# Kernel tuning notes

Measured on AMD Instinct MI355X. Metric: run time of the kernel, lower is better.

Reference implementation:

```python
import jax, jax.numpy as jnp
import numpy as np

PERIOD = 64
SCALE = 0.45


def setup_inputs() -> dict:
    key = jax.random.key(0)
    kq, kk, kv = jax.random.split(key, 3)
    B, L, D = 16, 8192, 512
    q = jax.random.normal(kq, (B, L, D), dtype=jnp.float32)
    k = jax.random.normal(kk, (B, L, D), dtype=jnp.float32)
    v = jax.random.normal(kv, (B, L, D), dtype=jnp.float32)
    return {"q": q, "k": k, "v": v}


def reference(q, k, v):
    # q, k, v: [B, L, D] with L % PERIOD == 0 and L == S, so the padding /
    # length-matching branches of the torch module are no-ops.
    B, L, D = q.shape
    nblk = L // PERIOD
    # permute to [B, D, L] then chunk the sequence into blocks of size PERIOD:
    # [B, D, nblk, PERIOD]. Attention is computed ACROSS blocks, with the
    # period dimension acting as the feature dimension.
    qb = q.transpose(0, 2, 1).reshape(B, D, nblk, PERIOD)
    kb = k.transpose(0, 2, 1).reshape(B, D, nblk, PERIOD)
    vb = v.transpose(0, 2, 1).reshape(B, D, nblk, PERIOD)
    # attn: [B, D, nblk, nblk]
    attn = jax.nn.softmax(jnp.einsum('bdnp,bdmp->bdnm', qb, kb) * SCALE, axis=-1)
    # out: [B, D, nblk, PERIOD] -> [B, D, L] -> [B, L, D]
    out = jnp.einsum('bdnm,bdmp->bdnp', attn, vb)
    out = out.reshape(B, D, L).transpose(0, 2, 1)
    return (out, attn)
```

## Files before the change

### kernel.cpp

```cpp
#include <hip/hip_runtime.h>
#include <stdint.h>

#define BB 16
#define LSEQ 8192
#define DD 512
#define PER 64
#define NBLK 128
#define QSCALE 0.45f

typedef __attribute__((ext_vector_type(8))) short short8;
typedef __attribute__((ext_vector_type(4))) float f32x4;
typedef __attribute__((ext_vector_type(2))) unsigned int uint2v;
typedef unsigned short ushort_t;

__device__ __forceinline__ ushort_t f2bf(float f) {
    union { float f; uint32_t u; } c; c.f = f;
    uint32_t u = c.u + 0x7FFFu + ((c.u >> 16) & 1u);
    return (ushort_t)(u >> 16);
}
__device__ __forceinline__ float bf2f(ushort_t h) {
    union { float f; uint32_t u; } c; c.u = ((uint32_t)h) << 16;
    return c.f;
}
__device__ __forceinline__ uint32_t pk2(float a, float b) {
    return (uint32_t)f2bf(a) | ((uint32_t)f2bf(b) << 16);
}

__global__ __launch_bounds__(256) void ktr(const float* __restrict__ q,
                                           const float* __restrict__ k,
                                           const float* __restrict__ v,
                                           ushort_t* __restrict__ qT,
                                           ushort_t* __restrict__ kT,
                                           ushort_t* __restrict__ vTT) {
    const int t = threadIdx.x;
    const int zz = blockIdx.z;
    const int role = zz >> 4;
    const int b = zz & (BB - 1);
    if (role < 2) {
        const float scale = role ? 1.0f : QSCALE;
        const float* sp = (role ? k : q) + (size_t)b * LSEQ * DD;
        ushort_t* dp = (role ? kT : qT) + (size_t)b * DD * LSEQ;
        const int l0 = blockIdx.x * 64 + 4 * (t & 15);
        const int d0 = blockIdx.y * 64 + 4 * (t >> 4);
        f32x4 vv[4];
#pragma unroll
        for (int j = 0; j < 4; ++j)
            vv[j] = __builtin_nontemporal_load(
                (const f32x4*)(sp + (size_t)(l0 + j) * DD + d0));
#pragma unroll
        for (int dj = 0; dj < 4; ++dj) {
            uint2v w;
            w[0] = pk2(vv[0][dj] * scale, vv[1][dj] * scale);
            w[1] = pk2(vv[2][dj] * scale, vv[3][dj] * scale);
            *(uint2v*)(dp + (size_t)(d0 + dj) * LSEQ + l0) = w;
        }
    } else {
        const int p = blockIdx.x & 63;
        const int mh = blockIdx.x >> 6;
        const int m0 = mh * 64 + 4 * (t & 15);
        const int d0 = blockIdx.y * 64 + 4 * (t >> 4);
        const float* vp = v + (size_t)b * LSEQ * DD;
        f32x4 x[4];
#pragma unroll
        for (int mj = 0; mj < 4; ++mj)
            x[mj] = __builtin_nontemporal_load(
                (const f32x4*)(vp + (size_t)((m0 + mj) * PER + p) * DD + d0));
#pragma unroll
        for (int dj = 0; dj < 4; ++dj) {
            uint2v w;
            w[0] = pk2(x[0][dj], x[1][dj]);
            w[1] = pk2(x[2][dj], x[3][dj]);
            *(uint2v*)(vTT + (size_t)((size_t)(b * DD + d0 + dj) * PER + p) * NBLK + m0) = w;
        }
    }
}

__global__ __launch_bounds__(256, 3) void katt(const ushort_t* __restrict__ qT,
                                               const ushort_t* __restrict__ kT,
                                               const ushort_t* __restrict__ vTT,
                                               float* __restrict__ attn,
                                               ushort_t* __restrict__ outT) {
    __shared__ __align__(16) ushort_t sm[24576];
    ushort_t* Qs = sm;
    ushort_t* Ks = sm + 8192;
    ushort_t* Ps = sm;
    ushort_t* Vs = sm + 16384;

    const int t = threadIdx.x;
    const int bd = blockIdx.x;
    const size_t base = (size_t)bd * 8192;
    const ushort_t* qp = qT + base;
    const ushort_t* kp = kT + base;
    const ushort_t* vp = vTT + base;

#pragma unroll
    for (int it = 0; it < 4; ++it) {
        int e = it * 2048 + t * 8;
        int n = e >> 6, pc = (e >> 3) & 7;
        int gq = pc ^ (n & 7);
        *(short8*)&Qs[n * 64 + gq * 8] = __builtin_nontemporal_load((const short8*)(qp + e));
        *(short8*)&Ks[n * 64 + gq * 8] = __builtin_nontemporal_load((const short8*)(kp + e));
        int p = e >> 7, mc = (e >> 3) & 15;
        int gv = mc ^ (p & 7);
        *(short8*)&Vs[p * 128 + gv * 8] = __builtin_nontemporal_load((const short8*)(vp + e));
    }
    __syncthreads();

    const int lane = t & 63, w = t >> 6;
    const int lrow = lane & 15, lquad = lane >> 4;

    f32x4 acc[2][8];
#pragma unroll
    for (int nt = 0; nt < 2; ++nt)
#pragma unroll
        for (int mt = 0; mt < 8; ++mt) acc[nt][mt] = (f32x4){0.f, 0.f, 0.f, 0.f};

    short8 aQ[2][2];
#pragma unroll
    for (int nt = 0; nt < 2; ++nt) {
        int n = w * 32 + nt * 16 + lrow;
#pragma unroll
        for (int s = 0; s < 2; ++s) {
            int g = (s * 4 + lquad) ^ (n & 7);
            aQ[nt][s] = *(const short8*)&Qs[n * 64 + g * 8];
        }
    }
#pragma unroll
    for (int mt = 0; mt < 8; ++mt) {
        int m = mt * 16 + lrow;
#pragma unroll
        for (int s = 0; s < 2; ++s) {
            int g = (s * 4 + lquad) ^ (m & 7);
            short8 bK = *(const short8*)&Ks[m * 64 + g * 8];
#pragma unroll
            for (int nt = 0; nt < 2; ++nt)
                acc[nt][mt] = __builtin_amdgcn_mfma_f32_16x16x32_bf16(aQ[nt][s], bK, acc[nt][mt], 0, 0, 0);
        }
    }
    __syncthreads();

    float* attnp = attn + (size_t)bd * (NBLK * NBLK);
#pragma unroll
    for (int nt = 0; nt < 2; ++nt) {
        int nbase = w * 32 + nt * 16;
#pragma unroll
        for (int r = 0; r < 4; ++r) {
            int row = nbase + lquad * 4 + r;
            float pv[8];
            float mx = -1e30f;
#pragma unroll
            for (int mt = 0; mt < 8; ++mt) { pv[mt] = acc[nt][mt][r]; mx = fmaxf(mx, pv[mt]); }
#pragma unroll
            for (int msk = 1; msk < 16; msk <<= 1) mx = fmaxf(mx, __shfl_xor(mx, msk, 64));
            float sum = 0.f;
#pragma unroll
            for (int mt = 0; mt < 8; ++mt) {
                pv[mt] = exp2f((pv[mt] - mx) * 1.4426950408889634f);
                sum += pv[mt];
            }
#pragma unroll
            for (int msk = 1; msk < 16; msk <<= 1) sum += __shfl_xor(sum, msk, 64);
            float inv = 1.0f / sum;
#pragma unroll
            for (int mt = 0; mt < 8; ++mt) {
                float a = pv[mt] * inv;
                int m = mt * 16 + lrow;
                __builtin_nontemporal_store(a, attnp + (size_t)row * NBLK + m);
                int g = (m >> 3) ^ (row & 7);
                Ps[row * 128 + g * 8 + (m & 7)] = f2bf(a);
            }
        }
    }

    f32x4 oacc[2][4];
#pragma unroll
    for (int nt = 0; nt < 2; ++nt)
#pragma unroll
        for (int pt = 0; pt < 4; ++pt) oacc[nt][pt] = (f32x4){0.f, 0.f, 0.f, 0.f};

#pragma unroll
    for (int s = 0; s < 4; ++s) {
        short8 aP[2];
#pragma unroll
        for (int nt = 0; nt < 2; ++nt) {
            int n = w * 32 + nt * 16 + lrow;
            int g = (s * 4 + lquad) ^ (n & 7);
            aP[nt] = *(const short8*)&Ps[n * 128 + g * 8];
        }
#pragma unroll
        for (int pt = 0; pt < 4; ++pt) {
            int prow = pt * 16 + lrow;
            int gv = (s * 4 + lquad) ^ (prow & 7);
            short8 bV = *(const short8*)&Vs[prow * 128 + gv * 8];
#pragma unroll
            for (int nt = 0; nt < 2; ++nt)
                oacc[nt][pt] = __builtin_amdgcn_mfma_f32_16x16x32_bf16(aP[nt], bV, oacc[nt][pt], 0, 0, 0);
        }
    }

    ushort_t* op = outT + base;
#pragma unroll
    for (int nt = 0; nt < 2; ++nt)
#pragma unroll
        for (int pt = 0; pt < 4; ++pt)
#pragma unroll
            for (int r = 0; r < 4; ++r) {
                int row = w * 32 + nt * 16 + lquad * 4 + r;
                int p = pt * 16 + lrow;
                op[row * PER + p] = f2bf(oacc[nt][pt][r]);
            }
}

__global__ __launch_bounds__(256) void ko(const ushort_t* __restrict__ outT,
                                          float* __restrict__ out) {
    const int t = threadIdx.x;
    const int l0 = blockIdx.x * 64 + 4 * (t & 15);
    const int d0 = blockIdx.y * 64 + 4 * (t >> 4);
    const int b = blockIdx.z;
    const ushort_t* sp = outT + (size_t)b * DD * LSEQ;
    float* op = out + (size_t)b * LSEQ * DD;
    uint2v ld[4];
#pragma unroll
    for (int dd = 0; dd < 4; ++dd)
        ld[dd] = __builtin_nontemporal_load(
            (const uint2v*)(sp + (size_t)(d0 + dd) * LSEQ + l0));
#pragma unroll
    for (int j = 0; j < 4; ++j) {
        f32x4 o;
#pragma unroll
        for (int dd = 0; dd < 4; ++dd)
            o[dd] = bf2f((ushort_t)((ld[dd][j >> 1] >> ((j & 1) * 16)) & 0xffffu));
        __builtin_nontemporal_store(o, (f32x4*)(op + (size_t)(l0 + j) * DD + d0));
    }
}

extern "C" void kernel_launch(void* const* d_in, const int* in_sizes, int n_in,
                              void* d_out, int out_size, void* d_ws, size_t ws_size,
                              hipStream_t stream) {
    const float* q = (const float*)d_in[0];
    const float* k = (const float*)d_in[1];
    const float* v = (const float*)d_in[2];
    float* outp = (float*)d_out;
    float* attnp = outp + (size_t)BB * LSEQ * DD;

    ushort_t* qT  = (ushort_t*)d_ws;
    ushort_t* kT  = qT  + (size_t)BB * DD * LSEQ;
    ushort_t* vTT = kT  + (size_t)BB * DD * LSEQ;
    ushort_t* oT  = vTT + (size_t)BB * DD * LSEQ;

    dim3 g1(LSEQ / 64, DD / 64, BB * 3);
    ktr<<<g1, 256, 0, stream>>>(q, k, v, qT, kT, vTT);
    katt<<<dim3(BB * DD), 256, 0, stream>>>(qT, kT, vTT, attnp, oT);
    dim3 g3(LSEQ / 64, DD / 64, BB);
    ko<<<g3, 256, 0, stream>>>(oT, outp);
}
```

Baseline: 494.3 us.

## Process batches in groups so bf16 workspace stays resident in cache

Splits the three-kernel pipeline into four sequential passes over groups of four batches, so the transposed bf16 Q/K/V and output workspace per pass is a quarter the size. It also switches nontemporal loads to normal loads so the intermediate data can stay in L2 or the infinity cache between kernels. The cost is more kernel launches and smaller grids per launch, which may reduce overlap and occupancy.

```diff
diff --git a/kernel.cpp b/kernel.cpp
--- a/kernel.cpp
+++ b/kernel.cpp
@@ -2,6 +2,8 @@
 #include <stdint.h>
 
 #define BB 16
+#define BG 4
+#define NG (BB / BG)
 #define LSEQ 8192
 #define DD 512
 #define PER 64
@@ -34,8 +36,8 @@
                                            ushort_t* __restrict__ vTT) {
     const int t = threadIdx.x;
     const int zz = blockIdx.z;
-    const int role = zz >> 4;
-    const int b = zz & (BB - 1);
+    const int role = zz >> 2;
+    const int b = zz & (BG - 1);
     if (role < 2) {
         const float scale = role ? 1.0f : QSCALE;
         const float* sp = (role ? k : q) + (size_t)b * LSEQ * DD;
@@ -98,11 +100,11 @@
         int e = it * 2048 + t * 8;
         int n = e >> 6, pc = (e >> 3) & 7;
         int gq = pc ^ (n & 7);
-        *(short8*)&Qs[n * 64 + gq * 8] = __builtin_nontemporal_load((const short8*)(qp + e));
-        *(short8*)&Ks[n * 64 + gq * 8] = __builtin_nontemporal_load((const short8*)(kp + e));
+        *(short8*)&Qs[n * 64 + gq * 8] = *(const short8*)(qp + e);
+        *(short8*)&Ks[n * 64 + gq * 8] = *(const short8*)(kp + e);
         int p = e >> 7, mc = (e >> 3) & 15;
         int gv = mc ^ (p & 7);
-        *(short8*)&Vs[p * 128 + gv * 8] = __builtin_nontemporal_load((const short8*)(vp + e));
+        *(short8*)&Vs[p * 128 + gv * 8] = *(const short8*)(vp + e);
     }
     __syncthreads();
 
@@ -222,8 +224,7 @@
     uint2v ld[4];
 #pragma unroll
     for (int dd = 0; dd < 4; ++dd)
-        ld[dd] = __builtin_nontemporal_load(
-            (const uint2v*)(sp + (size_t)(d0 + dd) * LSEQ + l0));
+        ld[dd] = *(const uint2v*)(sp + (size_t)(d0 + dd) * LSEQ + l0);
 #pragma unroll
     for (int j = 0; j < 4; ++j) {
         f32x4 o;
@@ -243,14 +244,24 @@
     float* outp = (float*)d_out;
     float* attnp = outp + (size_t)BB * LSEQ * DD;
 
+    const size_t perArr = (size_t)BG * DD * LSEQ;
     ushort_t* qT  = (ushort_t*)d_ws;
-    ushort_t* kT  = qT  + (size_t)BB * DD * LSEQ;
-    ushort_t* vTT = kT  + (size_t)BB * DD * LSEQ;
-    ushort_t* oT  = vTT + (size_t)BB * DD * LSEQ;
-
-    dim3 g1(LSEQ / 64, DD / 64, BB * 3);
-    ktr<<<g1, 256, 0, stream>>>(q, k, v, qT, kT, vTT);
-    katt<<<dim3(BB * DD), 256, 0, stream>>>(qT, kT, vTT, attnp, oT);
-    dim3 g3(LSEQ / 64, DD / 64, BB);
-    ko<<<g3, 256, 0, stream>>>(oT, outp);
-}
+    ushort_t* kT  = qT  + perArr;
+    ushort_t* vTT = kT  + perArr;
+    ushort_t* oT  = vTT + perArr;
+
+    const size_t inStride  = (size_t)BG * LSEQ * DD;
+    const size_t attStride = (size_t)BG * DD * NBLK * NBLK;
+
+    for (int g = 0; g < NG; ++g) {
+        const float* qg = q + (size_t)g * inStride;
+        const float* kg = k + (size_t)g * inStride;
+        const float* vg = v + (size_t)g * inStride;
+        dim3 g1(LSEQ / 64, DD / 64, BG * 3);
+        ktr<<<g1, 256, 0, stream>>>(qg, kg, vg, qT, kT, vTT);
+        katt<<<dim3(BG * DD), 256, 0, stream>>>(qT, kT, vTT,
+                                                attnp + (size_t)g * attStride, oT);
+        dim3 g3(LSEQ / 64, DD / 64, BG);
+        ko<<<g3, 256, 0, stream>>>(oT, outp + (size_t)g * inStride);
+    }
+}
```

Result: slower. 508.6 us (+2.9%).
